# Kernel tuning notes

Hardware: AMD Instinct MI355X
Metric: run time of the kernel (lower is better)

Reference implementation:

```python
import jax, jax.numpy as jnp
import numpy as np
import math

D = 512
BT = 4096
N = 16
EPS = 1e-5

def layer_norm(x, g, b):
    mu = jnp.mean(x, axis=-1, keepdims=True)
    var = jnp.mean(jnp.square(x - mu), axis=-1, keepdims=True)
    return (x - mu) * jax.lax.rsqrt(var + EPS) * g + b

def setup_inputs() -> dict:
    key = jax.random.key(0)
    ks = jax.random.split(key, 8)
    x = jax.random.normal(ks[0], (BT, N, D), dtype=jnp.float32)
    # random bool mask (True = masked), but keep the diagonal unmasked so no
    # row is fully -inf (avoids NaN softmax, matching sane usage of the module)
    attn_mask = jax.random.randint(ks[1], (BT, N, N), 0, 2).astype(bool)
    eye = jnp.eye(N, dtype=bool)[None, :, :]
    attn_mask = jnp.where(eye, False, attn_mask)
    # LayerNorm params (torch init: weight=1, bias=0)
    g1 = jnp.ones((D,), jnp.float32); b1 = jnp.zeros((D,), jnp.float32)
    g2 = jnp.ones((D,), jnp.float32); b2 = jnp.zeros((D,), jnp.float32)
    # FFN params: Linear(D, 4D) then Linear(4D, D)
    s1 = 1.0 / math.sqrt(D)
    s2 = 1.0 / math.sqrt(4 * D)
    W1 = jax.random.uniform(ks[2], (D, 4 * D), jnp.float32, -s1, s1)
    bW1 = jax.random.uniform(ks[3], (4 * D,), jnp.float32, -s1, s1)
    W2 = jax.random.uniform(ks[4], (4 * D, D), jnp.float32, -s2, s2)
    bW2 = jax.random.uniform(ks[5], (D,), jnp.float32, -s2, s2)
    return {"x": x, "attn_mask": attn_mask, "g1": g1, "b1": b1,
            "g2": g2, "b2": b2, "W1": W1, "bW1": bW1, "W2": W2, "bW2": bW2}

def reference(x, attn_mask, g1, b1, g2, b2, W1, bW1, W2, bW2):
    d = x.shape[-1]
    # scores: [BT, N, N] = x x^T / sqrt(d)
    scores = jnp.einsum('bnd,bmd->bnm', x, x) / jnp.sqrt(jnp.asarray(d, x.dtype))
    scores = jnp.where(attn_mask, -jnp.inf, scores)
    attn = jax.nn.softmax(scores, axis=-1)
    out = jnp.einsum('bnm,bmd->bnd', attn, x)
    h = layer_norm(x + out, g1, b1)
    ff = jnp.maximum(h @ W1 + bW1, 0.0) @ W2 + bW2
    y = layer_norm(h + ff, g2, b2)
    return y, attn
```

## Files before the change

### kernel.cpp

```cpp
#include <hip/hip_runtime.h>

typedef float  f32x4 __attribute__((ext_vector_type(4)));
typedef short  short8 __attribute__((ext_vector_type(8)));

__device__ __forceinline__ unsigned short f2bf(float f) {
    unsigned u = __builtin_bit_cast(unsigned, f);
    unsigned r = u + 0x7FFFu + ((u >> 16) & 1u);
    return (unsigned short)(r >> 16);
}
__device__ __forceinline__ float bf2f(unsigned short b) {
    return __builtin_bit_cast(float, (unsigned)b << 16);
}

__device__ __forceinline__ f32x4 mfma16(short8 a, short8 b, f32x4 c) {
    return __builtin_amdgcn_mfma_f32_16x16x32_bf16(a, b, c, 0, 0, 0);
}

#define GLOAD16(gp, lp) \
    __builtin_amdgcn_global_load_lds((const __attribute__((address_space(1))) unsigned int*)(gp), \
                                     (__attribute__((address_space(3))) unsigned int*)(lp), 16, 0, 0)

#define BT   4096
#define NTOK 16
#define DDIM 512
#define Y_ELEMS 33554432ULL
#define XS_STRIDE 516

__global__ __launch_bounds__(256) void transpose_kernel(const float* __restrict__ in,
                                                        unsigned short* __restrict__ out,
                                                        int R, int C) {
    __shared__ float tile[32][33];
    const int tx = threadIdx.x & 31, ty = threadIdx.x >> 5;
    const int c0 = blockIdx.x * 32, r0 = blockIdx.y * 32;
#pragma unroll
    for (int i = 0; i < 4; ++i)
        tile[ty + 8 * i][tx] = in[(size_t)(r0 + ty + 8 * i) * C + c0 + tx];
    __syncthreads();
#pragma unroll
    for (int i = 0; i < 4; ++i)
        out[(size_t)(c0 + ty + 8 * i) * R + r0 + tx] = f2bf(tile[tx][ty + 8 * i]);
}

__global__ void detect_kernel(const unsigned char* __restrict__ m, int* __restrict__ flag) {
    __shared__ int any;
    if (threadIdx.x == 0) any = 0;
    __syncthreads();
    int loc = 0;
    for (int i = threadIdx.x; i < 4096; i += 256)
        if (i & 3) loc |= m[i];
    if (loc) atomicOr(&any, 1);
    __syncthreads();
    if (threadIdx.x == 0) *flag = any ? 1 : 0;
}

__global__ __launch_bounds__(256) void stage1_kernel(
    const float* __restrict__ x,
    const unsigned char* __restrict__ mask_u8, const int* __restrict__ mask_i32,
    const int* __restrict__ flagp,
    const float* __restrict__ g1, const float* __restrict__ b1,
    float* __restrict__ attn_out, unsigned short* __restrict__ hbf) {
    __shared__ float xs[NTOK * XS_STRIDE];
    __shared__ float p_lds[256];

    const int b = blockIdx.x, t = threadIdx.x;
    const float* xb = x + (size_t)b * (NTOK * DDIM);

#pragma unroll
    for (int i = 0; i < 8; ++i) {
        int s = t + 256 * i;
        int r = s >> 7, c4 = s & 127;
        f32x4 v = ((const f32x4*)xb)[s];
        *(f32x4*)(&xs[r * XS_STRIDE + c4 * 4]) = v;
    }
    __syncthreads();

    const int r = t >> 4, c = t & 15;
    {
        const f32x4* xr = (const f32x4*)(&xs[r * XS_STRIDE]);
        const f32x4* xc = (const f32x4*)(&xs[c * XS_STRIDE]);
        f32x4 d4 = {0.f, 0.f, 0.f, 0.f};
#pragma unroll 8
        for (int u = 0; u < 128; ++u) d4 += xr[u] * xc[u];
        float s_rc = (d4.x + d4.y + d4.z + d4.w) * 0.04419417382415922f;

        const int flag = *flagp;
        size_t midx = (size_t)b * 256 + t;
        bool msk = flag ? (mask_u8[midx] != 0) : (mask_i32[midx] != 0);
        float sv = msk ? -1e30f : s_rc;
        float mx = sv;
        mx = fmaxf(mx, __shfl_xor(mx, 1, 16));
        mx = fmaxf(mx, __shfl_xor(mx, 2, 16));
        mx = fmaxf(mx, __shfl_xor(mx, 4, 16));
        mx = fmaxf(mx, __shfl_xor(mx, 8, 16));
        float e = msk ? 0.f : expf(sv - mx);
        float sum = e;
        sum += __shfl_xor(sum, 1, 16);
        sum += __shfl_xor(sum, 2, 16);
        sum += __shfl_xor(sum, 4, 16);
        sum += __shfl_xor(sum, 8, 16);
        float p = e / sum;
        p_lds[t] = p;
        attn_out[midx] = p;
    }
    __syncthreads();

    const int r2 = t >> 4, tc = t & 15;
    f32x4 acc[8];
#pragma unroll
    for (int j = 0; j < 8; ++j) acc[j] = (f32x4){0.f, 0.f, 0.f, 0.f};
    for (int c2 = 0; c2 < 16; ++c2) {
        float pw = p_lds[r2 * 16 + c2];
        const f32x4* xrow = (const f32x4*)(&xs[c2 * XS_STRIDE]);
#pragma unroll
        for (int j = 0; j < 8; ++j) acc[j] += pw * xrow[tc + 16 * j];
    }

    const f32x4* xme = (const f32x4*)(&xs[r2 * XS_STRIDE]);
    f32x4 vv[8];
    float s1 = 0.f, s2 = 0.f;
#pragma unroll
    for (int j = 0; j < 8; ++j) {
        f32x4 v = xme[tc + 16 * j] + acc[j];
        vv[j] = v;
        s1 += v.x + v.y + v.z + v.w;
        s2 += v.x * v.x + v.y * v.y + v.z * v.z + v.w * v.w;
    }
    s1 += __shfl_xor(s1, 1, 16); s2 += __shfl_xor(s2, 1, 16);
    s1 += __shfl_xor(s1, 2, 16); s2 += __shfl_xor(s2, 2, 16);
    s1 += __shfl_xor(s1, 4, 16); s2 += __shfl_xor(s2, 4, 16);
    s1 += __shfl_xor(s1, 8, 16); s2 += __shfl_xor(s2, 8, 16);
    float mu = s1 * (1.f / 512.f);
    float var = s2 * (1.f / 512.f) - mu * mu;
    float inv = rsqrtf(var + 1e-5f);

    unsigned short* hrow = hbf + (size_t)(b * NTOK + r2) * DDIM;
#pragma unroll
    for (int j = 0; j < 8; ++j) {
        int u = tc + 16 * j;
        f32x4 gv = ((const f32x4*)g1)[u];
        f32x4 bv = ((const f32x4*)b1)[u];
        f32x4 o = (vv[j] - mu) * inv * gv + bv;
        uint2 pk;
        pk.x = (unsigned)f2bf(o.x) | ((unsigned)f2bf(o.y) << 16);
        pk.y = (unsigned)f2bf(o.z) | ((unsigned)f2bf(o.w) << 16);
        *(uint2*)(hrow + u * 4) = pk;
    }
}

#define PH_READA(Al, Q) { short8 a00, a01, a10, a11; \
    a00 = *(const short8*)((Al) + aoffs[2*(Q)]   + kk2[0]); \
    a01 = *(const short8*)((Al) + aoffs[2*(Q)]   + kk2[1]); \
    a10 = *(const short8*)((Al) + aoffs[2*(Q)+1] + kk2[0]); \
    a11 = *(const short8*)((Al) + aoffs[2*(Q)+1] + kk2[1]);

#define PH_READB(Bl) \
    bb00 = *(const short8*)((Bl) + boffs[0] + kk2[0]); \
    bb01 = *(const short8*)((Bl) + boffs[0] + kk2[1]); \
    bb10 = *(const short8*)((Bl) + boffs[1] + kk2[0]); \
    bb11 = *(const short8*)((Bl) + boffs[1] + kk2[1]); \
    bb20 = *(const short8*)((Bl) + boffs[2] + kk2[0]); \
    bb21 = *(const short8*)((Bl) + boffs[2] + kk2[1]); \
    bb30 = *(const short8*)((Bl) + boffs[3] + kk2[0]); \
    bb31 = *(const short8*)((Bl) + boffs[3] + kk2[1]);

#define PH_MFMA(Q) \
    asm volatile("s_waitcnt lgkmcnt(0)" ::: "memory"); \
    __builtin_amdgcn_sched_barrier(0); \
    __builtin_amdgcn_s_setprio(1); \
    acc[2*(Q)][0]   = mfma16(a00, bb00, acc[2*(Q)][0]); \
    acc[2*(Q)][0]   = mfma16(a01, bb01, acc[2*(Q)][0]); \
    acc[2*(Q)][1]   = mfma16(a00, bb10, acc[2*(Q)][1]); \
    acc[2*(Q)][1]   = mfma16(a01, bb11, acc[2*(Q)][1]); \
    acc[2*(Q)][2]   = mfma16(a00, bb20, acc[2*(Q)][2]); \
    acc[2*(Q)][2]   = mfma16(a01, bb21, acc[2*(Q)][2]); \
    acc[2*(Q)][3]   = mfma16(a00, bb30, acc[2*(Q)][3]); \
    acc[2*(Q)][3]   = mfma16(a01, bb31, acc[2*(Q)][3]); \
    acc[2*(Q)+1][0] = mfma16(a10, bb00, acc[2*(Q)+1][0]); \
    acc[2*(Q)+1][0] = mfma16(a11, bb01, acc[2*(Q)+1][0]); \
    acc[2*(Q)+1][1] = mfma16(a10, bb10, acc[2*(Q)+1][1]); \
    acc[2*(Q)+1][1] = mfma16(a11, bb11, acc[2*(Q)+1][1]); \
    acc[2*(Q)+1][2] = mfma16(a10, bb20, acc[2*(Q)+1][2]); \
    acc[2*(Q)+1][2] = mfma16(a11, bb21, acc[2*(Q)+1][2]); \
    acc[2*(Q)+1][3] = mfma16(a10, bb30, acc[2*(Q)+1][3]); \
    acc[2*(Q)+1][3] = mfma16(a11, bb31, acc[2*(Q)+1][3]); \
    __builtin_amdgcn_s_setprio(0);

#define PH_END  __builtin_amdgcn_s_barrier(); }

#define GEMM_BODY(MORE) \
        PH_READA(A0lds, 0) PH_READB(B0lds) \
        stageA(v, A1lds, 0); stageA(v, A1lds, 1); \
        PH_MFMA(0) PH_END \
        PH_READA(A0lds, 1) \
        if (MORE) stageB(u2, B0lds, 0); \
        PH_MFMA(1) PH_END \
        PH_READA(A0lds, 2) \
        if (MORE) stageB(u2, B0lds, 1); \
        PH_MFMA(2) PH_END \
        PH_READA(A0lds, 3) \
        PH_MFMA(3) \
        if (MORE) { asm volatile("s_waitcnt vmcnt(4)" ::: "memory"); } \
        else      { asm volatile("s_waitcnt vmcnt(0)" ::: "memory"); } \
        PH_END \
        PH_READA(A1lds, 0) PH_READB(B1lds) \
        if (MORE) stageA(u2, A0lds, 0); \
        PH_MFMA(0) PH_END \
        PH_READA(A1lds, 1) \
        if (MORE) stageA(u2, A0lds, 1); \
        PH_MFMA(1) PH_END \
        PH_READA(A1lds, 2) \
        if (MORE) stageB(v2, B1lds, 0); \
        PH_MFMA(2) PH_END \
        PH_READA(A1lds, 3) \
        if (MORE) stageB(v2, B1lds, 1); \
        PH_MFMA(3) \
        if (MORE) { asm volatile("s_waitcnt vmcnt(4)" ::: "memory"); } \
        PH_END

__global__ __launch_bounds__(512, 2) void gemm1_kernel(
    const unsigned short* __restrict__ A, const unsigned short* __restrict__ Bw,
    const float* __restrict__ bias, unsigned short* __restrict__ Cbf) {
    constexpr int K = 512;
    constexpr int NT = K / 64;
    constexpr int NXT = 8;
    constexpr int NC = 2048;

    extern __shared__ unsigned short lds[];
    unsigned short* A0lds = lds;
    unsigned short* B0lds = lds + 16384;
    unsigned short* A1lds = lds + 32768;
    unsigned short* B1lds = lds + 49152;

    const int nwg = (int)gridDim.x;
    const int orig = (int)blockIdx.x;
    const int q8 = nwg >> 3, r8 = nwg & 7;
    const int xcd = orig & 7, idx = orig >> 3;
    const int w = (xcd < r8 ? xcd * (q8 + 1) : r8 * (q8 + 1) + (xcd - r8) * q8) + idx;
    const int mt_i = w / NXT, nt_i = w % NXT;
    const size_t arow0 = (size_t)mt_i * 256;
    const int n0 = nt_i * 256;

    const int tid = threadIdx.x;
    const int l = tid & 63, wv = tid >> 6;
    const int wm = wv >> 2, wn = wv & 3;
    const int lr = l & 15, lq = l >> 4;

    const int srow = tid >> 3;
    const int skb = ((((tid & 7) << 4) ^ ((srow & 7) << 4)) >> 1);

    const int sw = (lr & 7) << 4;
    int kk2[2];
    kk2[0] = ((lq * 16) ^ sw) >> 1;
    kk2[1] = ((64 + lq * 16) ^ sw) >> 1;
    int aoffs[8], boffs[4];
#pragma unroll
    for (int mf = 0; mf < 8; ++mf) aoffs[mf] = (wm * 128 + mf * 16 + lr) * 64;
#pragma unroll
    for (int nf = 0; nf < 4; ++nf) boffs[nf] = (wn * 64 + nf * 16 + lr) * 64;

    f32x4 acc[8][4];
#pragma unroll
    for (int i = 0; i < 8; ++i)
#pragma unroll
        for (int j = 0; j < 4; ++j) acc[i][j] = (f32x4){0.f, 0.f, 0.f, 0.f};

    short8 bb00, bb01, bb10, bb11, bb20, bb21, bb30, bb31;

    const unsigned short* Ath = A + (arow0 + srow) * (size_t)K + skb;
    const unsigned short* Bth = Bw + ((size_t)n0 + srow) * K + skb;

    auto stageA = [&](int tile, unsigned short* dst, int half) {
        const unsigned short* g = Ath + (size_t)half * (128 * K) + tile * 64;
        unsigned short* d = dst + half * 8192 + tid * 8;
        GLOAD16(g, d);
        GLOAD16(g + (size_t)64 * K, d + 4096);
    };
    auto stageB = [&](int tile, unsigned short* dst, int half) {
        const unsigned short* g = Bth + (size_t)half * (128 * K) + tile * 64;
        unsigned short* d = dst + half * 8192 + tid * 8;
        GLOAD16(g, d);
        GLOAD16(g + (size_t)64 * K, d + 4096);
    };

    stageB(0, B0lds, 0);
    stageB(0, B0lds, 1);
    stageA(0, A0lds, 0);
    stageA(0, A0lds, 1);
    stageB(1, B1lds, 0);
    stageB(1, B1lds, 1);
    asm volatile("s_waitcnt vmcnt(4)" ::: "memory");
    __builtin_amdgcn_s_barrier();

#pragma unroll 1
    for (int t = 0; t < NT / 2 - 1; ++t) {
        const int v = 2 * t + 1, u2 = 2 * t + 2, v2 = 2 * t + 3;
        GEMM_BODY(1)
    }
    {
        const int t = NT / 2 - 1;
        const int v = 2 * t + 1, u2 = 2 * t + 2, v2 = 2 * t + 3;
        (void)u2; (void)v2;
        GEMM_BODY(0)
    }

    float bv[4];
#pragma unroll
    for (int nf = 0; nf < 4; ++nf) bv[nf] = bias[n0 + wn * 64 + nf * 16 + lr];

#pragma unroll
    for (int mf = 0; mf < 8; ++mf) {
#pragma unroll
        for (int qq = 0; qq < 4; ++qq) {
            long row = (long)arow0 + wm * 128 + mf * 16 + lq * 4 + qq;
#pragma unroll
            for (int nf = 0; nf < 4; ++nf) {
                int col = n0 + wn * 64 + nf * 16 + lr;
                float vvv = acc[mf][nf][qq] + bv[nf];
                Cbf[(size_t)row * NC + col] = f2bf(fmaxf(vvv, 0.f));
            }
        }
    }
}


#define Q2_READB(Bl) \
    _Pragma("unroll") \
    for (int nf = 0; nf < 8; ++nf) { \
        bb[2 * nf]     = *(const short8*)((Bl) + boffs2[nf] + kk2[0]); \
        bb[2 * nf + 1] = *(const short8*)((Bl) + boffs2[nf] + kk2[1]); \
    }

#define Q2_PH(Al, Q) { short8 a0_, a1_; \
    a0_ = *(const short8*)((Al) + aoffs2[Q] + kk2[0]); \
    a1_ = *(const short8*)((Al) + aoffs2[Q] + kk2[1]);

#define Q2_MFMA(Q) \
    asm volatile("s_waitcnt lgkmcnt(0)" ::: "memory"); \
    __builtin_amdgcn_sched_barrier(0); \
    __builtin_amdgcn_s_setprio(1); \
    _Pragma("unroll") \
    for (int nf = 0; nf < 8; ++nf) { \
        acc[Q][nf] = mfma16(a0_, bb[2 * nf],     acc[Q][nf]); \
        acc[Q][nf] = mfma16(a1_, bb[2 * nf + 1], acc[Q][nf]); \
    } \
    __builtin_amdgcn_s_setprio(0);

#define Q2_END  __builtin_amdgcn_s_barrier(); }

#define BODY2(MORE) \
        Q2_READB(B0l) \
        Q2_PH(A0l, 0) stageA(v, A1l); Q2_MFMA(0) Q2_END \
        Q2_PH(A0l, 1) if (MORE) stageB(u2, B0l, 0); Q2_MFMA(1) Q2_END \
        Q2_PH(A0l, 2) if (MORE) stageB(u2, B0l, 1); Q2_MFMA(2) Q2_END \
        Q2_PH(A0l, 3) Q2_MFMA(3) \
        if (MORE) { asm volatile("s_waitcnt vmcnt(8)" ::: "memory"); } \
        else      { asm volatile("s_waitcnt vmcnt(0)" ::: "memory"); } \
        Q2_END \
        Q2_READB(B1l) \
        Q2_PH(A1l, 0) if (MORE) stageA(u2, A0l); Q2_MFMA(0) Q2_END \
        Q2_PH(A1l, 1) if (MORE) stageB(v2, B1l, 0); Q2_MFMA(1) Q2_END \
        Q2_PH(A1l, 2) if (MORE) stageB(v2, B1l, 1); Q2_MFMA(2) Q2_END \
        Q2_PH(A1l, 3) Q2_MFMA(3) \
        if (MORE) { asm volatile("s_waitcnt vmcnt(8)" ::: "memory"); } \
        Q2_END

__global__ __launch_bounds__(512, 2) void gemm2ln_kernel(
    const unsigned short* __restrict__ A,
    const unsigned short* __restrict__ Bw,
    const float* __restrict__ bias,
    const unsigned short* __restrict__ hres,
    const float* __restrict__ g2, const float* __restrict__ b2,
    float* __restrict__ y, long out_row0) {
    constexpr int K = 2048;
    constexpr int NT = K / 64;

    extern __shared__ unsigned short lds[];
    unsigned short* A0l = lds;
    unsigned short* A1l = lds + 8192;
    unsigned short* B0l = lds + 16384;
    unsigned short* B1l = lds + 49152;

    const int nwg = (int)gridDim.x;
    const int orig = (int)blockIdx.x;
    const int q8 = nwg >> 3, r8 = nwg & 7;
    const int xcd = orig & 7, idx = orig >> 3;
    const int w = (xcd < r8 ? xcd * (q8 + 1) : r8 * (q8 + 1) + (xcd - r8) * q8) + idx;
    const size_t arow0 = (size_t)w * 128;

    const int tid = threadIdx.x;
    const int l = tid & 63, wv = tid >> 6;
    const int wm = wv & 1, wn = wv >> 1;
    const int lr = l & 15, lq = l >> 4;

    const int srow = tid >> 3;
    const int skb = ((((tid & 7) << 4) ^ ((srow & 7) << 4)) >> 1);

    const int sw = (lr & 7) << 4;
    int kk2[2];
    kk2[0] = ((lq * 16) ^ sw) >> 1;
    kk2[1] = ((64 + lq * 16) ^ sw) >> 1;
    int aoffs2[4], boffs2[8];
#pragma unroll
    for (int mf = 0; mf < 4; ++mf) aoffs2[mf] = (wm * 64 + mf * 16 + lr) * 64;
#pragma unroll
    for (int nf = 0; nf < 8; ++nf) boffs2[nf] = (wn * 128 + nf * 16 + lr) * 64;

    f32x4 acc[4][8];
#pragma unroll
    for (int i = 0; i < 4; ++i)
#pragma unroll
        for (int j = 0; j < 8; ++j) acc[i][j] = (f32x4){0.f, 0.f, 0.f, 0.f};

    short8 bb[16];

    const unsigned short* Ath = A + (arow0 + srow) * (size_t)K + skb;
    const unsigned short* Bth = Bw + (size_t)srow * K + skb;

    auto stageA = [&](int tile, unsigned short* dst) {
        const unsigned short* g = Ath + tile * 64;
        unsigned short* d = dst + tid * 8;
        GLOAD16(g, d);
        GLOAD16(g + (size_t)64 * K, d + 4096);
    };
    auto stageB = [&](int tile, unsigned short* dst, int half) {
        const unsigned short* g = Bth + (size_t)(half * 256) * K + tile * 64;
        unsigned short* d = dst + half * 16384 + tid * 8;
#pragma unroll
        for (int i = 0; i < 4; ++i)
            GLOAD16(g + (size_t)(64 * i) * K, d + 4096 * i);
    };

    stageB(0, B0l, 0);
    stageB(0, B0l, 1);
    stageA(0, A0l);
    stageB(1, B1l, 0);
    stageB(1, B1l, 1);
    asm volatile("s_waitcnt vmcnt(8)" ::: "memory");
    __builtin_amdgcn_s_barrier();

#pragma unroll 1
    for (int t = 0; t < NT / 2 - 1; ++t) {
        const int v = 2 * t + 1, u2 = 2 * t + 2, v2 = 2 * t + 3;
        BODY2(1)
    }
    {
        const int t = NT / 2 - 1;
        const int v = 2 * t + 1, u2 = 2 * t + 2, v2 = 2 * t + 3;
        (void)u2; (void)v2;
        BODY2(0)
    }

    float* red = (float*)lds;
    float bv2[8], gv2[8], bb2[8];
#pragma unroll
    for (int nf = 0; nf < 8; ++nf) {
        int col = wn * 128 + nf * 16 + lr;
        bv2[nf] = bias[col];
        gv2[nf] = g2[col];
        bb2[nf] = b2[col];
    }

#pragma unroll
    for (int mf = 0; mf < 4; ++mf) {
#pragma unroll
        for (int qq = 0; qq < 4; ++qq) {
            int lrow = wm * 64 + mf * 16 + lq * 4 + qq;
            long grow = out_row0 + (long)arow0 + lrow;
            const unsigned short* hr = hres + (size_t)grow * 512 + wn * 128 + lr;
            float s = 0.f, s2 = 0.f;
#pragma unroll
            for (int nf = 0; nf < 8; ++nf) {
                float z = acc[mf][nf][qq] + bv2[nf] + bf2f(hr[nf * 16]);
                acc[mf][nf][qq] = z;
                s += z;
                s2 += z * z;
            }
            s += __shfl_xor(s, 1, 16); s2 += __shfl_xor(s2, 1, 16);
            s += __shfl_xor(s, 2, 16); s2 += __shfl_xor(s2, 2, 16);
            s += __shfl_xor(s, 4, 16); s2 += __shfl_xor(s2, 4, 16);
            s += __shfl_xor(s, 8, 16); s2 += __shfl_xor(s2, 8, 16);
            if (lr == 0) {
                red[wn * 128 + lrow] = s;
                red[512 + wn * 128 + lrow] = s2;
            }
        }
    }
    __syncthreads();

#pragma unroll
    for (int mf = 0; mf < 4; ++mf) {
#pragma unroll
        for (int qq = 0; qq < 4; ++qq) {
            int lrow = wm * 64 + mf * 16 + lq * 4 + qq;
            long grow = out_row0 + (long)arow0 + lrow;
            float s = red[lrow] + red[128 + lrow] + red[256 + lrow] + red[384 + lrow];
            float s2 = red[512 + lrow] + red[640 + lrow] + red[768 + lrow] + red[896 + lrow];
            float mu = s * (1.f / 512.f);
            float var = s2 * (1.f / 512.f) - mu * mu;
            float inv = rsqrtf(var + 1e-5f);
            float* yr = y + (size_t)grow * 512 + wn * 128 + lr;
#pragma unroll
            for (int nf = 0; nf < 8; ++nf)
                yr[nf * 16] = (acc[mf][nf][qq] - mu) * inv * gv2[nf] + bb2[nf];
        }
    }
}

extern "C" void kernel_launch(void* const* d_in, const int* in_sizes, int n_in,
                              void* d_out, int out_size, void* d_ws, size_t ws_size,
                              hipStream_t stream) {
    const float* x = (const float*)d_in[0];
    const void* mask = d_in[1];
    const float* g1 = (const float*)d_in[2];
    const float* b1 = (const float*)d_in[3];
    const float* g2 = (const float*)d_in[4];
    const float* b2 = (const float*)d_in[5];
    const float* W1 = (const float*)d_in[6];
    const float* bW1 = (const float*)d_in[7];
    const float* W2 = (const float*)d_in[8];
    const float* bW2 = (const float*)d_in[9];

    float* y = (float*)d_out;
    float* attn = y + Y_ELEMS;
    char* ws = (char*)d_ws;
    unsigned short* W1T = (unsigned short*)(ws);
    unsigned short* W2T = (unsigned short*)(ws + 2097152);
    int* flag = (int*)(ws + 4194304);
    unsigned short* h = (unsigned short*)(ws + 4194560);
    unsigned short* t1 = (unsigned short*)(ws + 71303424ULL);

    hipFuncSetAttribute((const void*)gemm1_kernel,
                        hipFuncAttributeMaxDynamicSharedMemorySize, 131072);
    hipFuncSetAttribute((const void*)gemm2ln_kernel,
                        hipFuncAttributeMaxDynamicSharedMemorySize, 163840);

    long cap256 = ((long)ws_size - 71303424L) / (256L * 2048L * 2L);
    if (cap256 < 1) cap256 = 1;
    if (cap256 > 256) cap256 = 256;

    transpose_kernel<<<dim3(64, 16), dim3(256), 0, stream>>>(W1, W1T, 512, 2048);
    transpose_kernel<<<dim3(16, 64), dim3(256), 0, stream>>>(W2, W2T, 2048, 512);
    detect_kernel<<<1, 256, 0, stream>>>((const unsigned char*)mask, flag);
    stage1_kernel<<<4096, 256, 0, stream>>>(x, (const unsigned char*)mask, (const int*)mask,
                                            flag, g1, b1, attn, h);
    for (long t0 = 0; t0 < 256; t0 += cap256) {
        long mt = (256 - t0 < cap256) ? (256 - t0) : cap256;
        long row0 = t0 * 256;
        gemm1_kernel<<<dim3((unsigned)(8 * mt)), 512, 131072, stream>>>(
            h + (size_t)row0 * 512, W1T, bW1, t1);
        gemm2ln_kernel<<<dim3((unsigned)(2 * mt)), 512, 163840, stream>>>(
            t1, W2T, bW2, h, g2, b2, y, row0);
    }
}
```

Measured before the change: 406.1 us.

## Hold A fragments in registers and stream B per phase in GEMM2

Reworks the GEMM2+LayerNorm main loop so each K-tile loads all four A fragments into registers once, then streams B in four quarter-phases of two n-fragments each, instead of preloading all of B and streaming A per phase. The prefetch schedule changes to match: A tiles are prefetched two ahead and B one ahead, with vmcnt waits adjusted to 2. This lowers the B register footprint, which could help register pressure, and changes the order of loads and MFMAs. The cost is a different LDS read pattern and a tighter prefetch distance for B, which risks stalls waiting on global memory.

```diff
diff --git a/kernel.cpp b/kernel.cpp
--- a/kernel.cpp
+++ b/kernel.cpp
@@ -323,46 +323,73 @@
 }
 
 
-#define Q2_READB(Bl) \
-    _Pragma("unroll") \
-    for (int nf = 0; nf < 8; ++nf) { \
-        bb[2 * nf]     = *(const short8*)((Bl) + boffs2[nf] + kk2[0]); \
-        bb[2 * nf + 1] = *(const short8*)((Bl) + boffs2[nf] + kk2[1]); \
-    }
-
-#define Q2_PH(Al, Q) { short8 a0_, a1_; \
-    a0_ = *(const short8*)((Al) + aoffs2[Q] + kk2[0]); \
-    a1_ = *(const short8*)((Al) + aoffs2[Q] + kk2[1]);
-
-#define Q2_MFMA(Q) \
+#define RD_A2(Al) \
+    areg[0][0] = *(const short8*)((Al) + aoffs2[0] + kk2[0]); \
+    areg[0][1] = *(const short8*)((Al) + aoffs2[0] + kk2[1]); \
+    areg[1][0] = *(const short8*)((Al) + aoffs2[1] + kk2[0]); \
+    areg[1][1] = *(const short8*)((Al) + aoffs2[1] + kk2[1]); \
+    areg[2][0] = *(const short8*)((Al) + aoffs2[2] + kk2[0]); \
+    areg[2][1] = *(const short8*)((Al) + aoffs2[2] + kk2[1]); \
+    areg[3][0] = *(const short8*)((Al) + aoffs2[3] + kk2[0]); \
+    areg[3][1] = *(const short8*)((Al) + aoffs2[3] + kk2[1]);
+
+#define RD_B2(Bl, q) \
+    bq00 = *(const short8*)((Bl) + boffs2[2*(q)]   + kk2[0]); \
+    bq01 = *(const short8*)((Bl) + boffs2[2*(q)]   + kk2[1]); \
+    bq10 = *(const short8*)((Bl) + boffs2[2*(q)+1] + kk2[0]); \
+    bq11 = *(const short8*)((Bl) + boffs2[2*(q)+1] + kk2[1]);
+
+#define MM_Q2(q) \
     asm volatile("s_waitcnt lgkmcnt(0)" ::: "memory"); \
     __builtin_amdgcn_sched_barrier(0); \
     __builtin_amdgcn_s_setprio(1); \
     _Pragma("unroll") \
-    for (int nf = 0; nf < 8; ++nf) { \
-        acc[Q][nf] = mfma16(a0_, bb[2 * nf],     acc[Q][nf]); \
-        acc[Q][nf] = mfma16(a1_, bb[2 * nf + 1], acc[Q][nf]); \
+    for (int mf = 0; mf < 4; ++mf) { \
+        acc[mf][2*(q)]   = mfma16(areg[mf][0], bq00, acc[mf][2*(q)]); \
+        acc[mf][2*(q)]   = mfma16(areg[mf][1], bq01, acc[mf][2*(q)]); \
+        acc[mf][2*(q)+1] = mfma16(areg[mf][0], bq10, acc[mf][2*(q)+1]); \
+        acc[mf][2*(q)+1] = mfma16(areg[mf][1], bq11, acc[mf][2*(q)+1]); \
     } \
     __builtin_amdgcn_s_setprio(0);
 
-#define Q2_END  __builtin_amdgcn_s_barrier(); }
+#define BAR2 __builtin_amdgcn_s_barrier();
 
 #define BODY2(MORE) \
-        Q2_READB(B0l) \
-        Q2_PH(A0l, 0) stageA(v, A1l); Q2_MFMA(0) Q2_END \
-        Q2_PH(A0l, 1) if (MORE) stageB(u2, B0l, 0); Q2_MFMA(1) Q2_END \
-        Q2_PH(A0l, 2) if (MORE) stageB(u2, B0l, 1); Q2_MFMA(2) Q2_END \
-        Q2_PH(A0l, 3) Q2_MFMA(3) \
-        if (MORE) { asm volatile("s_waitcnt vmcnt(8)" ::: "memory"); } \
+         \
+        RD_A2(A0l) RD_B2(B0l, 0) \
+        stageB(v, B1l, 0); \
+        MM_Q2(0) BAR2 \
+         \
+        RD_B2(B0l, 1) \
+        stageB(v, B1l, 1); \
+        if (MORE) stageA(u2, A0l); \
+        MM_Q2(1) BAR2 \
+         \
+        RD_B2(B0l, 2) \
+        MM_Q2(2) BAR2 \
+         \
+        RD_B2(B0l, 3) \
+        MM_Q2(3) \
+        if (MORE) { asm volatile("s_waitcnt vmcnt(2)" ::: "memory"); } \
         else      { asm volatile("s_waitcnt vmcnt(0)" ::: "memory"); } \
-        Q2_END \
-        Q2_READB(B1l) \
-        Q2_PH(A1l, 0) if (MORE) stageA(u2, A0l); Q2_MFMA(0) Q2_END \
-        Q2_PH(A1l, 1) if (MORE) stageB(v2, B1l, 0); Q2_MFMA(1) Q2_END \
-        Q2_PH(A1l, 2) if (MORE) stageB(v2, B1l, 1); Q2_MFMA(2) Q2_END \
-        Q2_PH(A1l, 3) Q2_MFMA(3) \
-        if (MORE) { asm volatile("s_waitcnt vmcnt(8)" ::: "memory"); } \
-        Q2_END
+        BAR2 \
+         \
+        RD_A2(A1l) RD_B2(B1l, 0) \
+        if (MORE) stageB(u2, B0l, 0); \
+        MM_Q2(0) BAR2 \
+         \
+        RD_B2(B1l, 1) \
+        if (MORE) { stageB(u2, B0l, 1); stageA(v2, A1l); } \
+        MM_Q2(1) BAR2 \
+         \
+        RD_B2(B1l, 2) \
+        MM_Q2(2) BAR2 \
+         \
+        RD_B2(B1l, 3) \
+        MM_Q2(3) \
+        if (MORE) { asm volatile("s_waitcnt vmcnt(2)" ::: "memory"); } \
+        else      { asm volatile("s_waitcnt vmcnt(0)" ::: "memory"); } \
+        BAR2
 
 __global__ __launch_bounds__(512, 2) void gemm2ln_kernel(
     const unsigned short* __restrict__ A,
@@ -411,7 +438,8 @@
 #pragma unroll
         for (int j = 0; j < 8; ++j) acc[i][j] = (f32x4){0.f, 0.f, 0.f, 0.f};
 
-    short8 bb[16];
+    short8 areg[4][2];
+    short8 bq00, bq01, bq10, bq11;
 
     const unsigned short* Ath = A + (arow0 + srow) * (size_t)K + skb;
     const unsigned short* Bth = Bw + (size_t)srow * K + skb;
@@ -430,12 +458,11 @@
             GLOAD16(g + (size_t)(64 * i) * K, d + 4096 * i);
     };
 
+    stageA(0, A0l);
     stageB(0, B0l, 0);
     stageB(0, B0l, 1);
-    stageA(0, A0l);
-    stageB(1, B1l, 0);
-    stageB(1, B1l, 1);
-    asm volatile("s_waitcnt vmcnt(8)" ::: "memory");
+    stageA(1, A1l);
+    asm volatile("s_waitcnt vmcnt(2)" ::: "memory");
     __builtin_amdgcn_s_barrier();
 
 #pragma unroll 1
```

Result: no change. 404.2 us (-0.5%).

## Rewrite gemm2ln main loop as simple 1024-thread double-buffered K=32 pipeline

Applied to the files above, without the earlier changes.

Replaces the hand-scheduled 512-thread gemm2+LayerNorm main loop, which used K=64 tiles, XOR-swizzled LDS, priority hints and explicit waitcnts, with a plain 1024-thread version. The new loop uses K=32 tiles, double buffering and a __syncthreads after every step. Each wave now computes a 64x64 sub-tile instead of 64x128, which halves accumulator registers per thread, and the LN reduction is extended to 8 column waves. The change drops the swizzle and the fine-grained scheduling, so it risks LDS bank conflicts and exposed load latency, plus more barriers per K. The LDS layout also changes, and the loop never waits on vmcnt explicitly before the barrier, so global-to-LDS loads may not be complete when they are read.

```diff
diff --git a/kernel.cpp b/kernel.cpp
--- a/kernel.cpp
+++ b/kernel.cpp
@@ -322,49 +322,7 @@
     }
 }
 
-
-#define Q2_READB(Bl) \
-    _Pragma("unroll") \
-    for (int nf = 0; nf < 8; ++nf) { \
-        bb[2 * nf]     = *(const short8*)((Bl) + boffs2[nf] + kk2[0]); \
-        bb[2 * nf + 1] = *(const short8*)((Bl) + boffs2[nf] + kk2[1]); \
-    }
-
-#define Q2_PH(Al, Q) { short8 a0_, a1_; \
-    a0_ = *(const short8*)((Al) + aoffs2[Q] + kk2[0]); \
-    a1_ = *(const short8*)((Al) + aoffs2[Q] + kk2[1]);
-
-#define Q2_MFMA(Q) \
-    asm volatile("s_waitcnt lgkmcnt(0)" ::: "memory"); \
-    __builtin_amdgcn_sched_barrier(0); \
-    __builtin_amdgcn_s_setprio(1); \
-    _Pragma("unroll") \
-    for (int nf = 0; nf < 8; ++nf) { \
-        acc[Q][nf] = mfma16(a0_, bb[2 * nf],     acc[Q][nf]); \
-        acc[Q][nf] = mfma16(a1_, bb[2 * nf + 1], acc[Q][nf]); \
-    } \
-    __builtin_amdgcn_s_setprio(0);
-
-#define Q2_END  __builtin_amdgcn_s_barrier(); }
-
-#define BODY2(MORE) \
-        Q2_READB(B0l) \
-        Q2_PH(A0l, 0) stageA(v, A1l); Q2_MFMA(0) Q2_END \
-        Q2_PH(A0l, 1) if (MORE) stageB(u2, B0l, 0); Q2_MFMA(1) Q2_END \
-        Q2_PH(A0l, 2) if (MORE) stageB(u2, B0l, 1); Q2_MFMA(2) Q2_END \
-        Q2_PH(A0l, 3) Q2_MFMA(3) \
-        if (MORE) { asm volatile("s_waitcnt vmcnt(8)" ::: "memory"); } \
-        else      { asm volatile("s_waitcnt vmcnt(0)" ::: "memory"); } \
-        Q2_END \
-        Q2_READB(B1l) \
-        Q2_PH(A1l, 0) if (MORE) stageA(u2, A0l); Q2_MFMA(0) Q2_END \
-        Q2_PH(A1l, 1) if (MORE) stageB(v2, B1l, 0); Q2_MFMA(1) Q2_END \
-        Q2_PH(A1l, 2) if (MORE) stageB(v2, B1l, 1); Q2_MFMA(2) Q2_END \
-        Q2_PH(A1l, 3) Q2_MFMA(3) \
-        if (MORE) { asm volatile("s_waitcnt vmcnt(8)" ::: "memory"); } \
-        Q2_END
-
-__global__ __launch_bounds__(512, 2) void gemm2ln_kernel(
+__global__ __launch_bounds__(1024) void gemm2ln_kernel(
     const unsigned short* __restrict__ A,
     const unsigned short* __restrict__ Bw,
     const float* __restrict__ bias,
@@ -372,13 +330,9 @@
     const float* __restrict__ g2, const float* __restrict__ b2,
     float* __restrict__ y, long out_row0) {
     constexpr int K = 2048;
-    constexpr int NT = K / 64;
+    constexpr int NT = K / 32;
 
     extern __shared__ unsigned short lds[];
-    unsigned short* A0l = lds;
-    unsigned short* A1l = lds + 8192;
-    unsigned short* B0l = lds + 16384;
-    unsigned short* B1l = lds + 49152;
 
     const int nwg = (int)gridDim.x;
     const int orig = (int)blockIdx.x;
@@ -389,72 +343,60 @@
 
     const int tid = threadIdx.x;
     const int l = tid & 63, wv = tid >> 6;
-    const int wm = wv & 1, wn = wv >> 1;
+    const int wm = wv >> 3, wn = wv & 7;
     const int lr = l & 15, lq = l >> 4;
 
-    const int srow = tid >> 3;
-    const int skb = ((((tid & 7) << 4) ^ ((srow & 7) << 4)) >> 1);
-
-    const int sw = (lr & 7) << 4;
-    int kk2[2];
-    kk2[0] = ((lq * 16) ^ sw) >> 1;
-    kk2[1] = ((64 + lq * 16) ^ sw) >> 1;
-    int aoffs2[4], boffs2[8];
-#pragma unroll
-    for (int mf = 0; mf < 4; ++mf) aoffs2[mf] = (wm * 64 + mf * 16 + lr) * 64;
-#pragma unroll
-    for (int nf = 0; nf < 8; ++nf) boffs2[nf] = (wn * 128 + nf * 16 + lr) * 64;
-
-    f32x4 acc[4][8];
+    int aoffs[4], boffs[4];
+#pragma unroll
+    for (int mf = 0; mf < 4; ++mf) aoffs[mf] = (wm * 64 + mf * 16 + lr) * 32 + lq * 8;
+#pragma unroll
+    for (int nf = 0; nf < 4; ++nf) boffs[nf] = (wn * 64 + nf * 16 + lr) * 32 + lq * 8;
+
+    f32x4 acc[4][4];
 #pragma unroll
     for (int i = 0; i < 4; ++i)
 #pragma unroll
-        for (int j = 0; j < 8; ++j) acc[i][j] = (f32x4){0.f, 0.f, 0.f, 0.f};
-
-    short8 bb[16];
-
-    const unsigned short* Ath = A + (arow0 + srow) * (size_t)K + skb;
-    const unsigned short* Bth = Bw + (size_t)srow * K + skb;
-
-    auto stageA = [&](int tile, unsigned short* dst) {
-        const unsigned short* g = Ath + tile * 64;
-        unsigned short* d = dst + tid * 8;
-        GLOAD16(g, d);
-        GLOAD16(g + (size_t)64 * K, d + 4096);
+        for (int j = 0; j < 4; ++j) acc[i][j] = (f32x4){0.f, 0.f, 0.f, 0.f};
+
+    const unsigned short* At = A + ((size_t)arow0 + (tid >> 2)) * K + (tid & 3) * 8;
+    const unsigned short* Bt = Bw + (size_t)(tid >> 2) * K + (tid & 3) * 8;
+
+    auto stage = [&](int t, int bi) {
+        if (tid < 512)
+            GLOAD16(At + t * 32, lds + bi * 4096 + tid * 8);
+        GLOAD16(Bt + t * 32, lds + 8192 + bi * 16384 + tid * 8);
+        GLOAD16(Bt + (size_t)256 * K + t * 32,
+                lds + 8192 + bi * 16384 + 8192 + tid * 8);
     };
-    auto stageB = [&](int tile, unsigned short* dst, int half) {
-        const unsigned short* g = Bth + (size_t)(half * 256) * K + tile * 64;
-        unsigned short* d = dst + half * 16384 + tid * 8;
-#pragma unroll
-        for (int i = 0; i < 4; ++i)
-            GLOAD16(g + (size_t)(64 * i) * K, d + 4096 * i);
-    };
-
-    stageB(0, B0l, 0);
-    stageB(0, B0l, 1);
-    stageA(0, A0l);
-    stageB(1, B1l, 0);
-    stageB(1, B1l, 1);
-    asm volatile("s_waitcnt vmcnt(8)" ::: "memory");
-    __builtin_amdgcn_s_barrier();
-
+
+    stage(0, 0);
+    __syncthreads();
+
+    int cur = 0;
 #pragma unroll 1
-    for (int t = 0; t < NT / 2 - 1; ++t) {
-        const int v = 2 * t + 1, u2 = 2 * t + 2, v2 = 2 * t + 3;
-        BODY2(1)
-    }
-    {
-        const int t = NT / 2 - 1;
-        const int v = 2 * t + 1, u2 = 2 * t + 2, v2 = 2 * t + 3;
-        (void)u2; (void)v2;
-        BODY2(0)
+    for (int t = 0; t < NT; ++t) {
+        if (t + 1 < NT) stage(t + 1, cur ^ 1);
+        const unsigned short* Ab = lds + cur * 4096;
+        const unsigned short* Bb = lds + 8192 + cur * 16384;
+        short8 af[4], bf4[4];
+#pragma unroll
+        for (int mf = 0; mf < 4; ++mf) af[mf] = *(const short8*)(Ab + aoffs[mf]);
+#pragma unroll
+        for (int nf = 0; nf < 4; ++nf) bf4[nf] = *(const short8*)(Bb + boffs[nf]);
+#pragma unroll
+        for (int mf = 0; mf < 4; ++mf)
+#pragma unroll
+            for (int nf = 0; nf < 4; ++nf)
+                acc[mf][nf] = mfma16(af[mf], bf4[nf], acc[mf][nf]);
+        __syncthreads();
+        cur ^= 1;
     }
 
     float* red = (float*)lds;
-    float bv2[8], gv2[8], bb2[8];
-#pragma unroll
-    for (int nf = 0; nf < 8; ++nf) {
-        int col = wn * 128 + nf * 16 + lr;
+    float bv2[4], gv2[4], bb2[4];
+#pragma unroll
+    for (int nf = 0; nf < 4; ++nf) {
+        int col = wn * 64 + nf * 16 + lr;
         bv2[nf] = bias[col];
         gv2[nf] = g2[col];
         bb2[nf] = b2[col];
@@ -466,10 +408,10 @@
         for (int qq = 0; qq < 4; ++qq) {
             int lrow = wm * 64 + mf * 16 + lq * 4 + qq;
             long grow = out_row0 + (long)arow0 + lrow;
-            const unsigned short* hr = hres + (size_t)grow * 512 + wn * 128 + lr;
+            const unsigned short* hr = hres + (size_t)grow * 512 + wn * 64 + lr;
             float s = 0.f, s2 = 0.f;
 #pragma unroll
-            for (int nf = 0; nf < 8; ++nf) {
+            for (int nf = 0; nf < 4; ++nf) {
                 float z = acc[mf][nf][qq] + bv2[nf] + bf2f(hr[nf * 16]);
                 acc[mf][nf][qq] = z;
                 s += z;
@@ -481,7 +423,7 @@
             s += __shfl_xor(s, 8, 16); s2 += __shfl_xor(s2, 8, 16);
             if (lr == 0) {
                 red[wn * 128 + lrow] = s;
-                red[512 + wn * 128 + lrow] = s2;
+                red[1024 + wn * 128 + lrow] = s2;
             }
         }
     }
@@ -493,14 +435,18 @@
         for (int qq = 0; qq < 4; ++qq) {
             int lrow = wm * 64 + mf * 16 + lq * 4 + qq;
             long grow = out_row0 + (long)arow0 + lrow;
-            float s = red[lrow] + red[128 + lrow] + red[256 + lrow] + red[384 + lrow];
-            float s2 = red[512 + lrow] + red[640 + lrow] + red[768 + lrow] + red[896 + lrow];
+            float s = 0.f, s2 = 0.f;
+#pragma unroll
+            for (int cc = 0; cc < 8; ++cc) {
+                s += red[cc * 128 + lrow];
+                s2 += red[1024 + cc * 128 + lrow];
+            }
             float mu = s * (1.f / 512.f);
             float var = s2 * (1.f / 512.f) - mu * mu;
             float inv = rsqrtf(var + 1e-5f);
-            float* yr = y + (size_t)grow * 512 + wn * 128 + lr;
-#pragma unroll
-            for (int nf = 0; nf < 8; ++nf)
+            float* yr = y + (size_t)grow * 512 + wn * 64 + lr;
+#pragma unroll
+            for (int nf = 0; nf < 4; ++nf)
                 yr[nf * 16] = (acc[mf][nf][qq] - mu) * inv * gv2[nf] + bb2[nf];
         }
     }
@@ -532,7 +478,7 @@
     hipFuncSetAttribute((const void*)gemm1_kernel,
                         hipFuncAttributeMaxDynamicSharedMemorySize, 131072);
     hipFuncSetAttribute((const void*)gemm2ln_kernel,
-                        hipFuncAttributeMaxDynamicSharedMemorySize, 163840);
+                        hipFuncAttributeMaxDynamicSharedMemorySize, 81920);
 
     long cap256 = ((long)ws_size - 71303424L) / (256L * 2048L * 2L);
     if (cap256 < 1) cap256 = 1;
@@ -548,7 +494,7 @@
         long row0 = t0 * 256;
         gemm1_kernel<<<dim3((unsigned)(8 * mt)), 512, 131072, stream>>>(
             h + (size_t)row0 * 512, W1T, bW1, t1);
-        gemm2ln_kernel<<<dim3((unsigned)(2 * mt)), 512, 163840, stream>>>(
+        gemm2ln_kernel<<<dim3((unsigned)(2 * mt)), 1024, 81920, stream>>>(
             t1, W2T, bW2, h, g2, b2, y, row0);
     }
 }
```

After: 464.6 us. 14.4% more time.
